# Performance work log

Hardware: AMD Instinct MI355X
Metric: run time of the kernel (lower is better)

The kernel has to match this reference:

```python
import jax, jax.numpy as jnp
import numpy as np

DIM = 192
HEADS = 6
WS = (4, 4, 4)
N = 64          # prod(WS)
NW = 64         # windows per sample
BATCH = 2048    # num_windows * B
CPB_HIDDEN = 512


def _make_rpb_tables():
    space = len(WS)
    coords = [np.arange(-(w - 1), w, dtype=np.float32) for w in WS]
    rpb = np.stack(np.meshgrid(*coords, indexing='ij'))  # (3, 7,7,7)
    for i in range(space):
        rpb[i] = rpb[i] / (WS[i] - 1)
    rpb = np.moveaxis(rpb, 0, -1)[None]  # (1,7,7,7,3)
    rpb = 8.0 * rpb
    rpb = np.sign(rpb) * np.log2(np.abs(rpb) + 1.0) / np.log2(8.0)
    grid = np.stack(np.meshgrid(*[np.arange(w) for w in WS], indexing='ij')).reshape(space, -1)  # (3, N)
    dists = grid[:, :, None] - grid[:, None, :]  # (3, N, N)
    for i in range(space):
        center = max(int(np.prod([2 * w - 1 for w in WS[i + 1:]])), 1)
        dists[i] = (dists[i] + WS[i] - 1) * center
    rpb_idx = dists.sum(0)  # (N, N), values in [0, 343)
    return jnp.asarray(rpb, jnp.float32), jnp.asarray(rpb_idx, jnp.int32)


def setup_inputs() -> dict:
    key = jax.random.key(0)
    ks = jax.random.split(key, 8)
    rpb, rpb_idx = _make_rpb_tables()
    s = 0.02
    return {
        'x': jax.random.normal(ks[0], (BATCH, N, DIM), jnp.float32),
        'mask': jnp.zeros((NW, N, N), jnp.float32),
        'rpb': rpb,
        'rpb_idx': rpb_idx,
        'cpb_w1': jax.random.normal(ks[1], (CPB_HIDDEN, len(WS)), jnp.float32) * s,
        'cpb_b1': jnp.zeros((CPB_HIDDEN,), jnp.float32),
        'cpb_w2': jax.random.normal(ks[2], (HEADS, CPB_HIDDEN), jnp.float32) * s,
        'qkv_w': jax.random.normal(ks[3], (3 * DIM, DIM), jnp.float32) * s,
        'qkv_b': jnp.zeros((3 * DIM,), jnp.float32),
        'proj_w': jax.random.normal(ks[4], (DIM, DIM), jnp.float32) * s,
        'proj_b': jnp.zeros((DIM,), jnp.float32),
        'logit_scale': jnp.log(10.0 * jnp.ones((HEADS, 1, 1), jnp.float32)),
    }


def reference(x, mask, rpb, rpb_idx, cpb_w1, cpb_b1, cpb_w2, qkv_w, qkv_b,
              proj_w, proj_b, logit_scale):
    B, n, C = x.shape
    H = logit_scale.shape[0]
    hd = C // H
    # qkv projection -> (3, B, H, n, hd)
    qkv = (x @ qkv_w.T + qkv_b).reshape(B, n, 3, H, hd).transpose(2, 0, 3, 1, 4)
    q, k, v = qkv[0], qkv[1], qkv[2]
    # continuous position bias MLP: (1,7,7,7,3) -> (1,7,7,7,H) -> gather -> (1,H,n,n)
    h1 = jax.nn.relu(rpb @ cpb_w1.T + cpb_b1)
    bias = (h1 @ cpb_w2.T).reshape(-1, H)            # (343, H)
    bias = bias[rpb_idx.reshape(-1)].reshape(n, n, H)
    bias = 16.0 * jax.nn.sigmoid(bias)
    bias = bias.transpose(2, 0, 1)[None]             # (1, H, n, n)
    # cosine attention
    qn = q / jnp.maximum(jnp.linalg.norm(q, axis=-1, keepdims=True), 1e-12)
    kn = k / jnp.maximum(jnp.linalg.norm(k, axis=-1, keepdims=True), 1e-12)
    scale = jnp.exp(jnp.minimum(logit_scale, jnp.log(jnp.float32(100.0))))  # clamp max=log(1/0.01)
    attn = jnp.einsum('bhnd,bhmd->bhnm', qn, kn) * scale + bias
    nW = mask.shape[0]
    attn = attn + jnp.tile(mask[:, None, :, :], (B // nW, 1, 1, 1))  # (B,1,n,n) broadcast over heads
    attn = jax.nn.softmax(attn, axis=-1)
    out = jnp.einsum('bhnm,bhmd->bhnd', attn, v)
    out = out.transpose(0, 2, 1, 3).reshape(B, n, C)  # heads-major concat (b n (h c))
    return out @ proj_w.T + proj_b
```

## Files before the change

kernel.cpp:

```cpp
#include <hip/hip_runtime.h>
#include <hip/hip_bf16.h>

#define DIM 192
#define HEADS 6
#define HD 32
#define NTOK 64
#define BATCH 2048
#define CPBH 512
#define TBL 343
#define NW 64

typedef unsigned int u32;
typedef __attribute__((ext_vector_type(8))) short b16x8;
typedef __attribute__((ext_vector_type(4))) float f32x4;

__device__ __forceinline__ unsigned short f2bf(float f) {
  union { __hip_bfloat16 h; unsigned short s; } cv;
  cv.h = __float2bfloat16(f);
  return cv.s;
}
__device__ __forceinline__ u32 pack2(float a, float b) {
  return (u32)f2bf(a) | ((u32)f2bf(b) << 16);
}
union FragU { u32 u[4]; b16x8 s; uint4 q; };

__device__ __forceinline__ b16x8 ld_frag_g(const u32* p) {
  FragU f; f.q = *(const uint4*)p; return f.s;
}

__global__ __launch_bounds__(64) void k_cpb1(
    const float* __restrict__ rpb, const float* __restrict__ w1,
    const float* __restrict__ b1, const float* __restrict__ w2,
    float* __restrict__ tab) {
  int t = blockIdx.x, lane = threadIdx.x;
  float r0 = rpb[t*3], r1 = rpb[t*3+1], r2 = rpb[t*3+2];
  float a[HEADS];
  #pragma unroll
  for (int h = 0; h < HEADS; ++h) a[h] = 0.f;
  #pragma unroll
  for (int kk = 0; kk < 8; ++kk) {
    int k = lane * 8 + kk;
    float hv = fmaf(r0, w1[k*3], fmaf(r1, w1[k*3+1], fmaf(r2, w1[k*3+2], b1[k])));
    hv = fmaxf(hv, 0.f);
    #pragma unroll
    for (int h = 0; h < HEADS; ++h) a[h] = fmaf(hv, w2[h*CPBH + k], a[h]);
  }
  #pragma unroll
  for (int h = 0; h < HEADS; ++h) {
    a[h] += __shfl_xor(a[h], 1);  a[h] += __shfl_xor(a[h], 2);
    a[h] += __shfl_xor(a[h], 4);  a[h] += __shfl_xor(a[h], 8);
    a[h] += __shfl_xor(a[h], 16); a[h] += __shfl_xor(a[h], 32);
  }
  if (lane == 0) {
    #pragma unroll
    for (int h = 0; h < HEADS; ++h) tab[t*HEADS + h] = a[h];
  }
}

__global__ void k_bm(const float* __restrict__ tab, const int* __restrict__ ridx,
                     const float* __restrict__ mask, float* __restrict__ bm) {
  int idx = blockIdx.x * blockDim.x + threadIdx.x;
  if (idx >= NW * HEADS * 4096) return;
  int ij = idx & 4095;
  int h = (idx >> 12) % HEADS;
  int nw = idx / (HEADS * 4096);
  float v = tab[ridx[ij] * HEADS + h];
  bm[idx] = 16.f / (1.f + __expf(-v)) + mask[nw * 4096 + ij];
}

__global__ void k_wcvt(const float* __restrict__ qkvw, const float* __restrict__ pw,
                       u32* __restrict__ wq, u32* __restrict__ wp) {
  int i = blockIdx.x * blockDim.x + threadIdx.x;
  if (i < 55296) {
    int R = i / 96, c = i % 96;
    int h  = R / 96;
    int t  = R - h * 96;
    int s3 = t >> 5;
    int u  = t & 31;
    int hf = (u >> 4) & 1;
    int p  = u & 15;
    int d  = ((p >> 2) << 3) + (hf << 2) + (p & 3);
    int orig = s3 * 192 + h * 32 + d;
    wq[i] = pack2(qkvw[orig*192 + 2*c], qkvw[orig*192 + 2*c + 1]);
  } else if (i < 55296 + 18432) {
    int j = i - 55296;
    wp[j] = pack2(pw[2*j], pw[2*j+1]);
  }
}

__global__ __launch_bounds__(384, 3) void k_fused(
    const float* __restrict__ x, const u32* __restrict__ wq,
    const float* __restrict__ qkvb, const float* __restrict__ bm,
    const float* __restrict__ ls, const u32* __restrict__ wp,
    const float* __restrict__ pb, float* __restrict__ out) {
  union ShU { u32 xl[NTOK * 101]; u32 aol[NTOK * 99]; };
  __shared__ ShU un;
  __shared__ u32 vTL[HEADS][32 * 35];
  __shared__ u32 pbt[HEADS][16 * 35];

  const int tid = threadIdx.x;
  const int b = blockIdx.x;
  const int h = tid >> 6;
  const int lane = tid & 63;
  const int m = lane & 15, qd = lane >> 4;

  {
    const float4* xg = (const float4*)(x + (size_t)b * (NTOK * DIM));
    for (int i = tid; i < (NTOK * DIM) / 4; i += 384) {
      float4 v = xg[i];
      int flat = i * 4, tok = flat / DIM, k = flat % DIM;
      un.xl[tok*101 + k/2]     = pack2(v.x, v.y);
      un.xl[tok*101 + k/2 + 1] = pack2(v.z, v.w);
    }
  }
  __syncthreads();

  b16x8 qfv[4], kfv[4];
  #pragma unroll
  for (int s3 = 0; s3 < 3; ++s3) {
    b16x8 afr[2][6];
    float bv[2][4];
    #pragma unroll
    for (int hf = 0; hf < 2; ++hf) {
      const u32* wrow = wq + (size_t)(((h*3 + s3)*2 + hf)*16 + m) * 96;
      #pragma unroll
      for (int ks = 0; ks < 6; ++ks) afr[hf][ks] = ld_frag_g(wrow + ks*16 + qd*4);
      #pragma unroll
      for (int r = 0; r < 4; ++r) bv[hf][r] = qkvb[s3*192 + h*32 + qd*8 + hf*4 + r];
    }
    #pragma unroll
    for (int t = 0; t < 4; ++t) {
      f32x4 a0 = {0.f,0.f,0.f,0.f}, a1 = {0.f,0.f,0.f,0.f};
      #pragma unroll
      for (int ks = 0; ks < 6; ++ks) {
        b16x8 bfr = *(const b16x8*)(&un.xl[(t*16 + m)*101 + ks*16 + qd*4]);
        a0 = __builtin_amdgcn_mfma_f32_16x16x32_bf16(afr[0][ks], bfr, a0, 0,0,0);
        a1 = __builtin_amdgcn_mfma_f32_16x16x32_bf16(afr[1][ks], bfr, a1, 0,0,0);
      }
      #pragma unroll
      for (int r = 0; r < 4; ++r) { a0[r] += bv[0][r]; a1[r] += bv[1][r]; }
      if (s3 < 2) {
        float ss = 0.f;
        #pragma unroll
        for (int r = 0; r < 4; ++r) ss = fmaf(a0[r],a0[r], fmaf(a1[r],a1[r], ss));
        ss += __shfl_xor(ss, 16);
        ss += __shfl_xor(ss, 32);
        float inv = 1.f / fmaxf(sqrtf(ss), 1e-12f);
        FragU tf;
        tf.u[0] = pack2(a0[0]*inv, a0[1]*inv);
        tf.u[1] = pack2(a0[2]*inv, a0[3]*inv);
        tf.u[2] = pack2(a1[0]*inv, a1[1]*inv);
        tf.u[3] = pack2(a1[2]*inv, a1[3]*inv);
        if (s3 == 0) qfv[t] = tf.s; else kfv[t] = tf.s;
      } else {
        float v8[8];
        #pragma unroll
        for (int r = 0; r < 4; ++r) { v8[r] = a0[r]; v8[4+r] = a1[r]; }
        #pragma unroll
        for (int e = 0; e < 8; ++e) {
          float pn = __shfl_xor(v8[e], 1);
          if ((m & 1) == 0) {
            int d = qd*8 + (e>>2)*4 + (e&3);
            vTL[h][d*35 + t*8 + (m>>1)] = pack2(v8[e], pn);
          }
        }
      }
    }
  }
  __syncthreads();

  const float sc = __expf(fminf(ls[h], 4.60517019f));
  const float* bmp = bm + ((size_t)(b & 63) * HEADS + h) * 4096;
  b16x8 vfr[2][2];
  #pragma unroll
  for (int nt = 0; nt < 2; ++nt)
    #pragma unroll
    for (int ks = 0; ks < 2; ++ks)
      vfr[nt][ks] = *(const b16x8*)(&vTL[h][(nt*16 + m)*35 + ks*16 + qd*4]);
  u32* pbw = pbt[h];
  #pragma unroll
  for (int mt = 0; mt < 4; ++mt) {
    f32x4 s4[4];
    #pragma unroll
    for (int ct = 0; ct < 4; ++ct) {
      f32x4 z = {0.f,0.f,0.f,0.f};
      s4[ct] = __builtin_amdgcn_mfma_f32_16x16x32_bf16(qfv[mt], kfv[ct], z, 0,0,0);
    }
    #pragma unroll
    for (int ct = 0; ct < 4; ++ct)
      #pragma unroll
      for (int r = 0; r < 4; ++r) {
        int row = mt*16 + qd*4 + r, col = ct*16 + m;
        s4[ct][r] = fmaf(s4[ct][r], sc, bmp[row*64 + col]);
      }
    float rinv[4];
    #pragma unroll
    for (int r = 0; r < 4; ++r) {
      float mm = s4[0][r];
      #pragma unroll
      for (int ct = 1; ct < 4; ++ct) mm = fmaxf(mm, s4[ct][r]);
      mm = fmaxf(mm, __shfl_xor(mm, 1)); mm = fmaxf(mm, __shfl_xor(mm, 2));
      mm = fmaxf(mm, __shfl_xor(mm, 4)); mm = fmaxf(mm, __shfl_xor(mm, 8));
      float l = 0.f;
      #pragma unroll
      for (int ct = 0; ct < 4; ++ct) { s4[ct][r] = __expf(s4[ct][r] - mm); l += s4[ct][r]; }
      l += __shfl_xor(l, 1); l += __shfl_xor(l, 2);
      l += __shfl_xor(l, 4); l += __shfl_xor(l, 8);
      rinv[r] = 1.f / l;
      int rloc = qd*4 + r;
      #pragma unroll
      for (int ct = 0; ct < 4; ++ct) {
        float pv = s4[ct][r];
        float pn = __shfl_xor(pv, 1);
        if ((m & 1) == 0) pbw[rloc*35 + ct*8 + (m >> 1)] = pack2(pv, pn);
      }
    }
    b16x8 pa0 = *(const b16x8*)(&pbw[m*35 + qd*4]);
    b16x8 pa1 = *(const b16x8*)(&pbw[m*35 + 16 + qd*4]);
    #pragma unroll
    for (int nt = 0; nt < 2; ++nt) {
      f32x4 o = {0.f,0.f,0.f,0.f};
      o = __builtin_amdgcn_mfma_f32_16x16x32_bf16(pa0, vfr[nt][0], o, 0,0,0);
      o = __builtin_amdgcn_mfma_f32_16x16x32_bf16(pa1, vfr[nt][1], o, 0,0,0);
      #pragma unroll
      for (int r = 0; r < 4; ++r) {
        float val = o[r] * rinv[r];
        float pn = __shfl_xor(val, 1);
        if ((m & 1) == 0)
          un.aol[(mt*16 + qd*4 + r)*99 + h*16 + nt*8 + (m >> 1)] = pack2(val, pn);
      }
    }
  }
  __syncthreads();

  const int wv = h;
  b16x8 pfr[2][6];
  float pbv[2][4];
  #pragma unroll
  for (int jj = 0; jj < 2; ++jj) {
    const u32* wrow = wp + (size_t)((wv*2 + jj)*16 + m) * 96;
    #pragma unroll
    for (int ks = 0; ks < 6; ++ks) pfr[jj][ks] = ld_frag_g(wrow + ks*16 + qd*4);
    #pragma unroll
    for (int r = 0; r < 4; ++r) pbv[jj][r] = pb[(wv*2 + jj)*16 + qd*4 + r];
  }
  #pragma unroll 1
  for (int t = 0; t < 4; ++t) {
    f32x4 acc0 = {0.f,0.f,0.f,0.f}, acc1 = {0.f,0.f,0.f,0.f};
    #pragma unroll
    for (int ks = 0; ks < 6; ++ks) {
      b16x8 bfr = *(const b16x8*)(&un.aol[(t*16 + m)*99 + ks*16 + qd*4]);
      acc0 = __builtin_amdgcn_mfma_f32_16x16x32_bf16(pfr[0][ks], bfr, acc0, 0,0,0);
      acc1 = __builtin_amdgcn_mfma_f32_16x16x32_bf16(pfr[1][ks], bfr, acc1, 0,0,0);
    }
    float* op = out + ((size_t)b*64 + t*16 + m) * DIM;
    *(float4*)(op + (wv*2+0)*16 + qd*4) =
        make_float4(acc0[0]+pbv[0][0], acc0[1]+pbv[0][1], acc0[2]+pbv[0][2], acc0[3]+pbv[0][3]);
    *(float4*)(op + (wv*2+1)*16 + qd*4) =
        make_float4(acc1[0]+pbv[1][0], acc1[1]+pbv[1][1], acc1[2]+pbv[1][2], acc1[3]+pbv[1][3]);
  }
}

extern "C" void kernel_launch(void* const* d_in, const int* in_sizes, int n_in,
                              void* d_out, int out_size, void* d_ws, size_t ws_size,
                              hipStream_t stream) {
  const float* x    = (const float*)d_in[0];
  const float* mask = (const float*)d_in[1];
  const float* rpb  = (const float*)d_in[2];
  const int*   ridx = (const int*)d_in[3];
  const float* w1   = (const float*)d_in[4];
  const float* b1   = (const float*)d_in[5];
  const float* w2   = (const float*)d_in[6];
  const float* qkvw = (const float*)d_in[7];
  const float* qkvb = (const float*)d_in[8];
  const float* pw   = (const float*)d_in[9];
  const float* pb   = (const float*)d_in[10];
  const float* ls   = (const float*)d_in[11];
  float* out = (float*)d_out;

  char* ws = (char*)d_ws;
  float* btab = (float*)(ws);
  float* bm   = (float*)(ws + 16384);
  u32* wq = (u32*)(ws + 16384 + 6291456);
  u32* wp = (u32*)(ws + 16384 + 6291456 + 221184);

  k_cpb1<<<TBL, 64, 0, stream>>>(rpb, w1, b1, w2, btab);
  k_wcvt<<<(73728 + 255) / 256, 256, 0, stream>>>(qkvw, pw, wq, wp);
  k_bm<<<(NW * HEADS * 4096 + 255) / 256, 256, 0, stream>>>(btab, ridx, mask, bm);
  k_fused<<<BATCH, 384, 0, stream>>>(x, wq, qkvb, bm, ls, wp, pb, out);
}
```

Baseline: 447.9 us.

## Alias shared buffers to raise occupancy, transpose bias table, merge prep kernels

Shared memory in the fused kernel is regrouped into two unions: x staging shares space with the probability buffer, and V-transpose shares space with the attention output. One extra barrier is added after V fragments are loaded so the regions can be reused safely. Launch bounds rise from 3 to 5 blocks per CU. The bias+mask table is stored column-major so each lane reads a float4 instead of four scalar gathers. The CPB MLP and weight-conversion kernels are merged into one launch. The risk is register pressure under the tighter bound and the cost of the added barrier.

```diff
diff --git a/kernel.cpp b/kernel.cpp
--- a/kernel.cpp
+++ b/kernel.cpp
@@ -28,49 +28,42 @@
   FragU f; f.q = *(const uint4*)p; return f.s;
 }
 
-__global__ __launch_bounds__(64) void k_cpb1(
+__global__ __launch_bounds__(256) void k_prep(
     const float* __restrict__ rpb, const float* __restrict__ w1,
     const float* __restrict__ b1, const float* __restrict__ w2,
-    float* __restrict__ tab) {
-  int t = blockIdx.x, lane = threadIdx.x;
-  float r0 = rpb[t*3], r1 = rpb[t*3+1], r2 = rpb[t*3+2];
-  float a[HEADS];
-  #pragma unroll
-  for (int h = 0; h < HEADS; ++h) a[h] = 0.f;
-  #pragma unroll
-  for (int kk = 0; kk < 8; ++kk) {
-    int k = lane * 8 + kk;
-    float hv = fmaf(r0, w1[k*3], fmaf(r1, w1[k*3+1], fmaf(r2, w1[k*3+2], b1[k])));
-    hv = fmaxf(hv, 0.f);
-    #pragma unroll
-    for (int h = 0; h < HEADS; ++h) a[h] = fmaf(hv, w2[h*CPBH + k], a[h]);
-  }
-  #pragma unroll
-  for (int h = 0; h < HEADS; ++h) {
-    a[h] += __shfl_xor(a[h], 1);  a[h] += __shfl_xor(a[h], 2);
-    a[h] += __shfl_xor(a[h], 4);  a[h] += __shfl_xor(a[h], 8);
-    a[h] += __shfl_xor(a[h], 16); a[h] += __shfl_xor(a[h], 32);
-  }
-  if (lane == 0) {
-    #pragma unroll
-    for (int h = 0; h < HEADS; ++h) tab[t*HEADS + h] = a[h];
-  }
-}
-
-__global__ void k_bm(const float* __restrict__ tab, const int* __restrict__ ridx,
-                     const float* __restrict__ mask, float* __restrict__ bm) {
-  int idx = blockIdx.x * blockDim.x + threadIdx.x;
-  if (idx >= NW * HEADS * 4096) return;
-  int ij = idx & 4095;
-  int h = (idx >> 12) % HEADS;
-  int nw = idx / (HEADS * 4096);
-  float v = tab[ridx[ij] * HEADS + h];
-  bm[idx] = 16.f / (1.f + __expf(-v)) + mask[nw * 4096 + ij];
-}
-
-__global__ void k_wcvt(const float* __restrict__ qkvw, const float* __restrict__ pw,
-                       u32* __restrict__ wq, u32* __restrict__ wp) {
-  int i = blockIdx.x * blockDim.x + threadIdx.x;
+    float* __restrict__ tab,
+    const float* __restrict__ qkvw, const float* __restrict__ pw,
+    u32* __restrict__ wq, u32* __restrict__ wp) {
+  const int tid = threadIdx.x;
+  if (blockIdx.x < 88) {
+    int t = blockIdx.x * 4 + (tid >> 6);
+    int lane = tid & 63;
+    if (t >= TBL) return;
+    float r0 = rpb[t*3], r1 = rpb[t*3+1], r2 = rpb[t*3+2];
+    float a[HEADS];
+    #pragma unroll
+    for (int h = 0; h < HEADS; ++h) a[h] = 0.f;
+    #pragma unroll
+    for (int kk = 0; kk < 8; ++kk) {
+      int k = lane * 8 + kk;
+      float hv = fmaf(r0, w1[k*3], fmaf(r1, w1[k*3+1], fmaf(r2, w1[k*3+2], b1[k])));
+      hv = fmaxf(hv, 0.f);
+      #pragma unroll
+      for (int h = 0; h < HEADS; ++h) a[h] = fmaf(hv, w2[h*CPBH + k], a[h]);
+    }
+    #pragma unroll
+    for (int h = 0; h < HEADS; ++h) {
+      a[h] += __shfl_xor(a[h], 1);  a[h] += __shfl_xor(a[h], 2);
+      a[h] += __shfl_xor(a[h], 4);  a[h] += __shfl_xor(a[h], 8);
+      a[h] += __shfl_xor(a[h], 16); a[h] += __shfl_xor(a[h], 32);
+    }
+    if (lane == 0) {
+      #pragma unroll
+      for (int h = 0; h < HEADS; ++h) tab[t*HEADS + h] = a[h];
+    }
+    return;
+  }
+  int i = (blockIdx.x - 88) * 256 + tid;
   if (i < 55296) {
     int R = i / 96, c = i % 96;
     int h  = R / 96;
@@ -88,15 +81,29 @@
   }
 }
 
-__global__ __launch_bounds__(384, 3) void k_fused(
+__global__ void k_bm(const float* __restrict__ tab, const int* __restrict__ ridx,
+                     const float* __restrict__ mask, float* __restrict__ bm) {
+  int idx = blockIdx.x * blockDim.x + threadIdx.x;
+  if (idx >= NW * HEADS * 4096) return;
+  int row = idx & 63;
+  int col = (idx >> 6) & 63;
+  int h = (idx >> 12) % HEADS;
+  int nw = idx / (HEADS * 4096);
+  int ij = row * 64 + col;
+  float v = tab[ridx[ij] * HEADS + h];
+  bm[idx] = 16.f / (1.f + __expf(-v)) + mask[nw * 4096 + ij];
+}
+
+union RegA { u32 xl[NTOK * 101]; u32 pbt[HEADS][16 * 35]; };
+union RegB { u32 vTL[HEADS][32 * 35]; u32 aol[NTOK * 99]; };
+
+__global__ __launch_bounds__(384, 5) void k_fused(
     const float* __restrict__ x, const u32* __restrict__ wq,
     const float* __restrict__ qkvb, const float* __restrict__ bm,
     const float* __restrict__ ls, const u32* __restrict__ wp,
     const float* __restrict__ pb, float* __restrict__ out) {
-  union ShU { u32 xl[NTOK * 101]; u32 aol[NTOK * 99]; };
-  __shared__ ShU un;
-  __shared__ u32 vTL[HEADS][32 * 35];
-  __shared__ u32 pbt[HEADS][16 * 35];
+  __shared__ RegA rA;
+  __shared__ RegB rB;
 
   const int tid = threadIdx.x;
   const int b = blockIdx.x;
@@ -109,8 +116,8 @@
     for (int i = tid; i < (NTOK * DIM) / 4; i += 384) {
       float4 v = xg[i];
       int flat = i * 4, tok = flat / DIM, k = flat % DIM;
-      un.xl[tok*101 + k/2]     = pack2(v.x, v.y);
-      un.xl[tok*101 + k/2 + 1] = pack2(v.z, v.w);
+      rA.xl[tok*101 + k/2]     = pack2(v.x, v.y);
+      rA.xl[tok*101 + k/2 + 1] = pack2(v.z, v.w);
     }
   }
   __syncthreads();
@@ -133,7 +140,7 @@
       f32x4 a0 = {0.f,0.f,0.f,0.f}, a1 = {0.f,0.f,0.f,0.f};
       #pragma unroll
       for (int ks = 0; ks < 6; ++ks) {
-        b16x8 bfr = *(const b16x8*)(&un.xl[(t*16 + m)*101 + ks*16 + qd*4]);
+        b16x8 bfr = *(const b16x8*)(&rA.xl[(t*16 + m)*101 + ks*16 + qd*4]);
         a0 = __builtin_amdgcn_mfma_f32_16x16x32_bf16(afr[0][ks], bfr, a0, 0,0,0);
         a1 = __builtin_amdgcn_mfma_f32_16x16x32_bf16(afr[1][ks], bfr, a1, 0,0,0);
       }
@@ -161,7 +168,7 @@
           float pn = __shfl_xor(v8[e], 1);
           if ((m & 1) == 0) {
             int d = qd*8 + (e>>2)*4 + (e&3);
-            vTL[h][d*35 + t*8 + (m>>1)] = pack2(v8[e], pn);
+            rB.vTL[h][d*35 + t*8 + (m>>1)] = pack2(v8[e], pn);
           }
         }
       }
@@ -169,15 +176,17 @@
   }
   __syncthreads();
 
-  const float sc = __expf(fminf(ls[h], 4.60517019f));
-  const float* bmp = bm + ((size_t)(b & 63) * HEADS + h) * 4096;
   b16x8 vfr[2][2];
   #pragma unroll
   for (int nt = 0; nt < 2; ++nt)
     #pragma unroll
     for (int ks = 0; ks < 2; ++ks)
-      vfr[nt][ks] = *(const b16x8*)(&vTL[h][(nt*16 + m)*35 + ks*16 + qd*4]);
-  u32* pbw = pbt[h];
+      vfr[nt][ks] = *(const b16x8*)(&rB.vTL[h][(nt*16 + m)*35 + ks*16 + qd*4]);
+  __syncthreads();
+
+  const float sc = __expf(fminf(ls[h], 4.60517019f));
+  const float* bmp = bm + ((size_t)(b & 63) * HEADS + h) * 4096;
+  u32* pbw = rA.pbt[h];
   #pragma unroll
   for (int mt = 0; mt < 4; ++mt) {
     f32x4 s4[4];
@@ -187,12 +196,13 @@
       s4[ct] = __builtin_amdgcn_mfma_f32_16x16x32_bf16(qfv[mt], kfv[ct], z, 0,0,0);
     }
     #pragma unroll
-    for (int ct = 0; ct < 4; ++ct)
-      #pragma unroll
-      for (int r = 0; r < 4; ++r) {
-        int row = mt*16 + qd*4 + r, col = ct*16 + m;
-        s4[ct][r] = fmaf(s4[ct][r], sc, bmp[row*64 + col]);
-      }
+    for (int ct = 0; ct < 4; ++ct) {
+      float4 b4 = *(const float4*)(bmp + (ct*16 + m)*64 + mt*16 + qd*4);
+      s4[ct][0] = fmaf(s4[ct][0], sc, b4.x);
+      s4[ct][1] = fmaf(s4[ct][1], sc, b4.y);
+      s4[ct][2] = fmaf(s4[ct][2], sc, b4.z);
+      s4[ct][3] = fmaf(s4[ct][3], sc, b4.w);
+    }
     float rinv[4];
     #pragma unroll
     for (int r = 0; r < 4; ++r) {
@@ -227,7 +237,7 @@
         float val = o[r] * rinv[r];
         float pn = __shfl_xor(val, 1);
         if ((m & 1) == 0)
-          un.aol[(mt*16 + qd*4 + r)*99 + h*16 + nt*8 + (m >> 1)] = pack2(val, pn);
+          rB.aol[(mt*16 + qd*4 + r)*99 + h*16 + nt*8 + (m >> 1)] = pack2(val, pn);
       }
     }
   }
@@ -249,7 +259,7 @@
     f32x4 acc0 = {0.f,0.f,0.f,0.f}, acc1 = {0.f,0.f,0.f,0.f};
     #pragma unroll
     for (int ks = 0; ks < 6; ++ks) {
-      b16x8 bfr = *(const b16x8*)(&un.aol[(t*16 + m)*99 + ks*16 + qd*4]);
+      b16x8 bfr = *(const b16x8*)(&rB.aol[(t*16 + m)*99 + ks*16 + qd*4]);
       acc0 = __builtin_amdgcn_mfma_f32_16x16x32_bf16(pfr[0][ks], bfr, acc0, 0,0,0);
       acc1 = __builtin_amdgcn_mfma_f32_16x16x32_bf16(pfr[1][ks], bfr, acc1, 0,0,0);
     }
@@ -284,8 +294,7 @@
   u32* wq = (u32*)(ws + 16384 + 6291456);
   u32* wp = (u32*)(ws + 16384 + 6291456 + 221184);
 
-  k_cpb1<<<TBL, 64, 0, stream>>>(rpb, w1, b1, w2, btab);
-  k_wcvt<<<(73728 + 255) / 256, 256, 0, stream>>>(qkvw, pw, wq, wp);
+  k_prep<<<376, 256, 0, stream>>>(rpb, w1, b1, w2, btab, qkvw, pw, wq, wp);
   k_bm<<<(NW * HEADS * 4096 + 255) / 256, 256, 0, stream>>>(btab, ridx, mask, bm);
   k_fused<<<BATCH, 384, 0, stream>>>(x, wq, qkvb, bm, ls, wp, pb, out);
 }
```

Measured after the change: 575.7 us. 28.5% more time.
